# Kernel tuning notes

Hardware: AMD Instinct MI355X
Metric: run time of the kernel (lower is better)

## Reference

```python
import jax, jax.numpy as jnp
import numpy as np

HID = 128
SCALE = np.sqrt(HID)


def _ln(x, g, b, eps=1e-5):
    m = jnp.mean(x, axis=-1, keepdims=True)
    v = jnp.mean((x - m) ** 2, axis=-1, keepdims=True)
    return (x - m) * jax.lax.rsqrt(v + eps) * g + b


def _attention(img, txt, Wi, bi, Wt, bt, g1, b1, Wq, bq, Wk, bk, Wv, bv, g2, b2, Wo, bo):
    # img: [..., S, image_dim], txt: [..., S, text_dim] -> [..., S, HID]
    c = img @ Wi.T + bi + txt @ Wt.T + bt
    c = _ln(c, g1, b1)
    q = c @ Wq.T + bq
    k = c @ Wk.T + bk
    v = c @ Wv.T + bv
    s = jnp.einsum('...qd,...kd->...qk', q, k) / (SCALE + 1e-8)
    a = jax.nn.softmax(s, axis=-1)
    a = a + 1e-10
    a = a / jnp.sum(a, axis=-1, keepdims=True)
    a = jnp.clip(a, 1e-7, 1.0)
    ctx = jnp.einsum('...qk,...kd->...qd', a, v)
    ctx = _ln(ctx, g2, b2)
    return ctx @ Wo.T + bo


def setup_inputs() -> dict:
    key = jax.random.key(0)
    ks = jax.random.split(key, 24)
    T, Q, DI, DT = 256, 64, 2048, 768

    def xavier(k, shape):
        fan_in, fan_out = shape[1], shape[0]
        lim = np.sqrt(6.0 / (fan_in + fan_out))
        return jax.random.uniform(k, shape, jnp.float32, -lim, lim)

    return {
        'support_images': jax.random.normal(ks[0], (T, 4, DI), jnp.float32),
        'support_texts': jax.random.normal(ks[1], (T, 4, DT), jnp.float32),
        'support_labels': jax.random.randint(ks[2], (T, 4), 0, 4, jnp.int64),
        'query_images': jax.random.normal(ks[3], (T, Q, DI), jnp.float32),
        'query_texts': jax.random.normal(ks[4], (T, Q, DT), jnp.float32),
        'Wi': xavier(ks[5], (HID, DI)), 'bi': jnp.zeros((HID,)),
        'Wt': xavier(ks[6], (HID, DT)), 'bt': jnp.zeros((HID,)),
        'g1': jnp.ones((HID,)), 'b1': jnp.zeros((HID,)),
        'Wq': xavier(ks[7], (HID, HID)), 'bq': jnp.zeros((HID,)),
        'Wk': xavier(ks[8], (HID, HID)), 'bk': jnp.zeros((HID,)),
        'Wv': xavier(ks[9], (HID, HID)), 'bv': jnp.zeros((HID,)),
        'g2': jnp.ones((HID,)), 'b2': jnp.zeros((HID,)),
        'Wo': xavier(ks[10], (HID, HID)), 'bo': jnp.zeros((HID,)),
    }


def reference(support_images, support_texts, support_labels, query_images, query_texts,
              Wi, bi, Wt, bt, g1, b1, Wq, bq, Wk, bk, Wv, bv, g2, b2, Wo, bo):
    p = (Wi, bi, Wt, bt, g1, b1, Wq, bq, Wk, bk, Wv, bv, g2, b2, Wo, bo)
    # Support: attention across the 4 support items of each task -> [T, 4, HID]
    support_feats = _attention(support_images, support_texts, *p)
    # Queries: source processes each query alone (seq len 1) -> add singleton seq axis
    qf = _attention(query_images[:, :, None, :], query_texts[:, :, None, :], *p)
    qf = qf[:, :, 0, :]  # [T, Q, HID]
    # Cosine-similarity prototype scoring (eps=1e-8 as in F.cosine_similarity)
    qn = qf / jnp.clip(jnp.linalg.norm(qf, axis=-1, keepdims=True), 1e-8, None)
    pn = support_feats / jnp.clip(jnp.linalg.norm(support_feats, axis=-1, keepdims=True), 1e-8, None)
    logits = jnp.einsum('tqd,tcd->tqc', qn, pn) * 10.0  # [T, Q, 4]
    return logits
```

## Files before the change

### kernel.cpp

```cpp
#include <hip/hip_runtime.h>

typedef __bf16 bf16_t;
typedef __attribute__((ext_vector_type(4))) __bf16 bf16x4;
typedef __attribute__((ext_vector_type(8))) __bf16 bf16x8;
typedef __attribute__((ext_vector_type(4))) float floatx4;

#define LN_EPS 1e-5f

__global__ __launch_bounds__(256) void k0_init(
    const float* __restrict__ bi, const float* __restrict__ bt,
    float* __restrict__ c_all)
{
    int i = blockIdx.x * 256 + threadIdx.x;
    int c4 = i & 31;
    float4 a = ((const float4*)bi)[c4];
    float4 b = ((const float4*)bt)[c4];
    float4 v; v.x = a.x + b.x; v.y = a.y + b.y; v.z = a.z + b.z; v.w = a.w + b.w;
    ((float4*)c_all)[i] = v;
}

#define K1_SA 72
#define K1_SB 72

__global__ __launch_bounds__(256) void k1_gemm(
    const float* __restrict__ qimg, const float* __restrict__ qtxt,
    const float* __restrict__ simg, const float* __restrict__ stxt,
    const float* __restrict__ Wi,   const float* __restrict__ Wt,
    float* __restrict__ c_all)
{
    __shared__ bf16_t lA[64 * K1_SA];
    __shared__ bf16_t lB[128 * K1_SB];

    const int tid  = threadIdx.x;
    const int m0   = blockIdx.x * 64;
    const int chnk = blockIdx.y;
    const bool isq = (m0 < 16384);
    const int rb   = isq ? m0 : (m0 - 16384);
    const float* Aimg = isq ? qimg : simg;
    const float* Atxt = isq ? qtxt : stxt;

    const int wid  = tid >> 6;
    const int lane = tid & 63;
    const int quad = lane >> 4;
    const int l16  = lane & 15;
    const int wr   = wid >> 1;
    const int wc   = wid & 1;

    const int arow = tid >> 2, acol = (tid & 3) * 4;

    floatx4 acc[2][4];
#pragma unroll
    for (int i = 0; i < 2; ++i)
#pragma unroll
        for (int j = 0; j < 4; ++j) acc[i][j] = (floatx4)0.f;

    for (int s = 0; s < 11; ++s) {
        const int k0 = chnk * 704 + s * 64;
        const float* abase; const float* bbase; size_t lda, ldb;
        if (k0 < 2048) {
            abase = Aimg + (size_t)rb * 2048 + k0; lda = 2048;
            bbase = Wi + k0;                        ldb = 2048;
        } else {
            abase = Atxt + (size_t)rb * 768 + (k0 - 2048); lda = 768;
            bbase = Wt + (k0 - 2048);                       ldb = 768;
        }
        __syncthreads();
        {
            const float* p = abase + (size_t)arow * lda + acol;
#pragma unroll
            for (int j = 0; j < 4; ++j) {
                float4 v = *(const float4*)(p + 16 * j);
                bf16x4 pk; pk.x = (bf16_t)v.x; pk.y = (bf16_t)v.y;
                           pk.z = (bf16_t)v.z; pk.w = (bf16_t)v.w;
                *(bf16x4*)&lA[arow * K1_SA + acol + 16 * j] = pk;
            }
        }
#pragma unroll
        for (int pp = 0; pp < 2; ++pp) {
            int brow = pp * 64 + (tid >> 2);
            const float* p = bbase + (size_t)brow * ldb + acol;
#pragma unroll
            for (int j = 0; j < 4; ++j) {
                float4 v = *(const float4*)(p + 16 * j);
                bf16x4 pk; pk.x = (bf16_t)v.x; pk.y = (bf16_t)v.y;
                           pk.z = (bf16_t)v.z; pk.w = (bf16_t)v.w;
                *(bf16x4*)&lB[brow * K1_SB + acol + 16 * j] = pk;
            }
        }
        __syncthreads();
#pragma unroll
        for (int ks = 0; ks < 2; ++ks) {
            bf16x8 af[2], bfr[4];
#pragma unroll
            for (int mt = 0; mt < 2; ++mt)
                af[mt] = *(const bf16x8*)&lA[(wr * 32 + mt * 16 + l16) * K1_SA + ks * 32 + quad * 8];
#pragma unroll
            for (int nt = 0; nt < 4; ++nt)
                bfr[nt] = *(const bf16x8*)&lB[(wc * 64 + nt * 16 + l16) * K1_SB + ks * 32 + quad * 8];
#pragma unroll
            for (int mt = 0; mt < 2; ++mt)
#pragma unroll
                for (int nt = 0; nt < 4; ++nt)
                    acc[mt][nt] = __builtin_amdgcn_mfma_f32_16x16x32_bf16(
                        af[mt], bfr[nt], acc[mt][nt], 0, 0, 0);
        }
    }
#pragma unroll
    for (int nt = 0; nt < 4; ++nt) {
        int col = wc * 64 + nt * 16 + l16;
#pragma unroll
        for (int mt = 0; mt < 2; ++mt)
#pragma unroll
            for (int r = 0; r < 4; ++r) {
                int row = wr * 32 + mt * 16 + quad * 4 + r;
                unsafeAtomicAdd(&c_all[(size_t)(m0 + row) * 128 + col], acc[mt][nt][r]);
            }
    }
}

#define K2_ST 136

__global__ __launch_bounds__(256) void k2_query(
    const float* __restrict__ c_all,
    const float* __restrict__ Wv, const float* __restrict__ bv,
    const float* __restrict__ Wo, const float* __restrict__ bo,
    const float* __restrict__ g1, const float* __restrict__ b1,
    const float* __restrict__ g2, const float* __restrict__ b2,
    float* __restrict__ qn)
{
    __shared__ bf16_t tT[64 * K2_ST];
    __shared__ bf16_t tW[128 * K2_ST];

    const int tid  = threadIdx.x;
    const int wid  = tid >> 6;
    const int lane = tid & 63;
    const int quad = lane >> 4;
    const int l16  = lane & 15;
    const int t0   = blockIdx.x * 64;
    const int r0   = wid * 16;

    float bvr[8], g2r[8], b2r[8], bor[8];
#pragma unroll
    for (int nt = 0; nt < 8; ++nt) {
        int col = nt * 16 + l16;
        bvr[nt] = bv[col]; g2r[nt] = g2[col]; b2r[nt] = b2[col]; bor[nt] = bo[col];
    }
    const float g1l = g1[lane], g1h = g1[64 + lane];
    const float b1l = b1[lane], b1h = b1[64 + lane];

    for (int i = 0; i < 16; ++i) {
        int row = r0 + i;
        const float* src = c_all + (size_t)(t0 + row) * 128;
        float x0 = src[lane], x1 = src[64 + lane];
        float s = x0 + x1, q = x0 * x0 + x1 * x1;
#pragma unroll
        for (int m = 1; m < 64; m <<= 1) { s += __shfl_xor(s, m); q += __shfl_xor(q, m); }
        float mean = s * (1.f / 128.f);
        float var  = q * (1.f / 128.f) - mean * mean;
        float rs   = rsqrtf(var + LN_EPS);
        tT[row * K2_ST + lane]      = (bf16_t)((x0 - mean) * rs * g1l + b1l);
        tT[row * K2_ST + 64 + lane] = (bf16_t)((x1 - mean) * rs * g1h + b1h);
    }
#pragma unroll
    for (int i = 0; i < 16; ++i) {
        int idx = i * 1024 + tid * 4;
        int r = idx >> 7, cc = idx & 127;
        float4 v = *(const float4*)(Wv + idx);
        bf16x4 pk; pk.x = (bf16_t)v.x; pk.y = (bf16_t)v.y;
                   pk.z = (bf16_t)v.z; pk.w = (bf16_t)v.w;
        *(bf16x4*)&tW[r * K2_ST + cc] = pk;
    }
    __syncthreads();

    floatx4 acc[8];
#pragma unroll
    for (int nt = 0; nt < 8; ++nt) acc[nt] = (floatx4)0.f;
#pragma unroll
    for (int ks = 0; ks < 4; ++ks) {
        bf16x8 a = *(const bf16x8*)&tT[(r0 + l16) * K2_ST + ks * 32 + quad * 8];
#pragma unroll
        for (int nt = 0; nt < 8; ++nt) {
            bf16x8 b = *(const bf16x8*)&tW[(nt * 16 + l16) * K2_ST + ks * 32 + quad * 8];
            acc[nt] = __builtin_amdgcn_mfma_f32_16x16x32_bf16(a, b, acc[nt], 0, 0, 0);
        }
    }
#pragma unroll
    for (int nt = 0; nt < 8; ++nt)
#pragma unroll
        for (int r = 0; r < 4; ++r) acc[nt][r] += bvr[nt];

#pragma unroll
    for (int r = 0; r < 4; ++r) {
        float s = 0.f, q = 0.f;
#pragma unroll
        for (int nt = 0; nt < 8; ++nt) { float x = acc[nt][r]; s += x; q += x * x; }
#pragma unroll
        for (int m = 1; m < 16; m <<= 1) { s += __shfl_xor(s, m); q += __shfl_xor(q, m); }
        float mean = s * (1.f / 128.f);
        float var  = q * (1.f / 128.f) - mean * mean;
        float rs   = rsqrtf(var + LN_EPS);
        int row = r0 + quad * 4 + r;
#pragma unroll
        for (int nt = 0; nt < 8; ++nt) {
            float y = (acc[nt][r] - mean) * rs * g2r[nt] + b2r[nt];
            tT[row * K2_ST + nt * 16 + l16] = (bf16_t)y;
        }
    }
    __syncthreads();
#pragma unroll
    for (int i = 0; i < 16; ++i) {
        int idx = i * 1024 + tid * 4;
        int r = idx >> 7, cc = idx & 127;
        float4 v = *(const float4*)(Wo + idx);
        bf16x4 pk; pk.x = (bf16_t)v.x; pk.y = (bf16_t)v.y;
                   pk.z = (bf16_t)v.z; pk.w = (bf16_t)v.w;
        *(bf16x4*)&tW[r * K2_ST + cc] = pk;
    }
    __syncthreads();

#pragma unroll
    for (int nt = 0; nt < 8; ++nt) acc[nt] = (floatx4)0.f;
#pragma unroll
    for (int ks = 0; ks < 4; ++ks) {
        bf16x8 a = *(const bf16x8*)&tT[(r0 + l16) * K2_ST + ks * 32 + quad * 8];
#pragma unroll
        for (int nt = 0; nt < 8; ++nt) {
            bf16x8 b = *(const bf16x8*)&tW[(nt * 16 + l16) * K2_ST + ks * 32 + quad * 8];
            acc[nt] = __builtin_amdgcn_mfma_f32_16x16x32_bf16(a, b, acc[nt], 0, 0, 0);
        }
    }
#pragma unroll
    for (int r = 0; r < 4; ++r) {
        float q = 0.f;
#pragma unroll
        for (int nt = 0; nt < 8; ++nt) {
            float x = acc[nt][r] + bor[nt]; acc[nt][r] = x; q += x * x;
        }
#pragma unroll
        for (int m = 1; m < 16; m <<= 1) q += __shfl_xor(q, m);
        float inv = 1.f / fmaxf(sqrtf(q), 1e-8f);
        int row = t0 + r0 + quad * 4 + r;
#pragma unroll
        for (int nt = 0; nt < 8; ++nt)
            qn[(size_t)row * 128 + nt * 16 + l16] = acc[nt][r] * inv;
    }
}

__global__ __launch_bounds__(256) void k3_support(
    const float* __restrict__ c_all,
    const float* __restrict__ Wq, const float* __restrict__ bq,
    const float* __restrict__ Wk, const float* __restrict__ bk,
    const float* __restrict__ Wv, const float* __restrict__ bv,
    const float* __restrict__ Wo, const float* __restrict__ bo,
    const float* __restrict__ g1, const float* __restrict__ b1,
    const float* __restrict__ g2, const float* __restrict__ b2,
    float* __restrict__ pn)
{
    __shared__ float  cs[4][128];
    __shared__ bf16_t tW[128 * K2_ST];
    __shared__ float  qkv[3][4][128];
    __shared__ float  att[4][4];
    __shared__ float  ctx[4][128];

    const int tid  = threadIdx.x;
    const int wid  = tid >> 6;
    const int lane = tid & 63;
    const int task = blockIdx.x;

    {
        const float* src = c_all + (size_t)(16384 + task * 4 + wid) * 128;
        float x0 = src[lane], x1 = src[64 + lane];
        float s = x0 + x1, q = x0 * x0 + x1 * x1;
#pragma unroll
        for (int m = 1; m < 64; m <<= 1) { s += __shfl_xor(s, m); q += __shfl_xor(q, m); }
        float mean = s * (1.f / 128.f);
        float var  = q * (1.f / 128.f) - mean * mean;
        float rs   = rsqrtf(var + LN_EPS);
        cs[wid][lane]      = (x0 - mean) * rs * g1[lane] + b1[lane];
        cs[wid][64 + lane] = (x1 - mean) * rs * g1[64 + lane] + b1[64 + lane];
    }

    const float* Ws[3] = { Wq, Wk, Wv };
    const float* Bs[3] = { bq, bk, bv };
    for (int w = 0; w < 3; ++w) {
        __syncthreads();
#pragma unroll
        for (int i = 0; i < 16; ++i) {
            int idx = i * 1024 + tid * 4;
            int r = idx >> 7, cc = idx & 127;
            float4 v = *(const float4*)(Ws[w] + idx);
            bf16x4 pk; pk.x = (bf16_t)v.x; pk.y = (bf16_t)v.y;
                       pk.z = (bf16_t)v.z; pk.w = (bf16_t)v.w;
            *(bf16x4*)&tW[r * K2_ST + cc] = pk;
        }
        __syncthreads();
#pragma unroll
        for (int j = 0; j < 2; ++j) {
            int o = tid + j * 256;
            int s = o >> 7, n = o & 127;
            const float4* c4 = (const float4*)cs[s];
            float acc = 0.f;
#pragma unroll
            for (int k8 = 0; k8 < 16; ++k8) {
                bf16x8 wv = *(const bf16x8*)&tW[n * K2_ST + k8 * 8];
                float4 a0 = c4[k8 * 2], a1 = c4[k8 * 2 + 1];
                acc += a0.x * (float)wv[0] + a0.y * (float)wv[1]
                     + a0.z * (float)wv[2] + a0.w * (float)wv[3]
                     + a1.x * (float)wv[4] + a1.y * (float)wv[5]
                     + a1.z * (float)wv[6] + a1.w * (float)wv[7];
            }
            qkv[w][s][n] = acc + Bs[w][n];
        }
    }
    __syncthreads();
    if (tid < 16) {
        int i = tid >> 2, j = tid & 3;
        const float4* qv = (const float4*)qkv[0][i];
        const float4* kv = (const float4*)qkv[1][j];
        float acc = 0.f;
#pragma unroll
        for (int k = 0; k < 32; ++k) {
            float4 a = qv[k], b = kv[k];
            acc += a.x * b.x + a.y * b.y + a.z * b.z + a.w * b.w;
        }
        att[i][j] = acc * (float)(1.0 / (11.313708498984761 + 1e-8));
    }
    __syncthreads();
    if (tid < 4) {
        float s0 = att[tid][0], s1 = att[tid][1], s2 = att[tid][2], s3 = att[tid][3];
        float m = fmaxf(fmaxf(s0, s1), fmaxf(s2, s3));
        float e0 = expf(s0 - m), e1 = expf(s1 - m), e2 = expf(s2 - m), e3 = expf(s3 - m);
        float se = e0 + e1 + e2 + e3;
        float a0 = e0 / se + 1e-10f, a1 = e1 / se + 1e-10f;
        float a2 = e2 / se + 1e-10f, a3 = e3 / se + 1e-10f;
        float t = a0 + a1 + a2 + a3;
        att[tid][0] = fminf(fmaxf(a0 / t, 1e-7f), 1.f);
        att[tid][1] = fminf(fmaxf(a1 / t, 1e-7f), 1.f);
        att[tid][2] = fminf(fmaxf(a2 / t, 1e-7f), 1.f);
        att[tid][3] = fminf(fmaxf(a3 / t, 1e-7f), 1.f);
    }
    __syncthreads();
#pragma unroll
    for (int j = 0; j < 2; ++j) {
        int o = tid + j * 256;
        int s = o >> 7, n = o & 127;
        ctx[s][n] = att[s][0] * qkv[2][0][n] + att[s][1] * qkv[2][1][n]
                  + att[s][2] * qkv[2][2][n] + att[s][3] * qkv[2][3][n];
    }
    __syncthreads();
    {
        float x0 = ctx[wid][lane], x1 = ctx[wid][64 + lane];
        float s = x0 + x1, q = x0 * x0 + x1 * x1;
#pragma unroll
        for (int m = 1; m < 64; m <<= 1) { s += __shfl_xor(s, m); q += __shfl_xor(q, m); }
        float mean = s * (1.f / 128.f);
        float var  = q * (1.f / 128.f) - mean * mean;
        float rs   = rsqrtf(var + LN_EPS);
        cs[wid][lane]      = (x0 - mean) * rs * g2[lane] + b2[lane];
        cs[wid][64 + lane] = (x1 - mean) * rs * g2[64 + lane] + b2[64 + lane];
    }
    __syncthreads();
#pragma unroll
    for (int i = 0; i < 16; ++i) {
        int idx = i * 1024 + tid * 4;
        int r = idx >> 7, cc = idx & 127;
        float4 v = *(const float4*)(Wo + idx);
        bf16x4 pk; pk.x = (bf16_t)v.x; pk.y = (bf16_t)v.y;
                   pk.z = (bf16_t)v.z; pk.w = (bf16_t)v.w;
        *(bf16x4*)&tW[r * K2_ST + cc] = pk;
    }
    __syncthreads();
#pragma unroll
    for (int j = 0; j < 2; ++j) {
        int o = tid + j * 256;
        int s = o >> 7, n = o & 127;
        const float4* c4 = (const float4*)cs[s];
        float acc = 0.f;
#pragma unroll
        for (int k8 = 0; k8 < 16; ++k8) {
            bf16x8 wv = *(const bf16x8*)&tW[n * K2_ST + k8 * 8];
            float4 a0 = c4[k8 * 2], a1 = c4[k8 * 2 + 1];
            acc += a0.x * (float)wv[0] + a0.y * (float)wv[1]
                 + a0.z * (float)wv[2] + a0.w * (float)wv[3]
                 + a1.x * (float)wv[4] + a1.y * (float)wv[5]
                 + a1.z * (float)wv[6] + a1.w * (float)wv[7];
        }
        ctx[s][n] = acc + bo[n];
    }
    __syncthreads();
    {
        float x0 = ctx[wid][lane], x1 = ctx[wid][64 + lane];
        float q = x0 * x0 + x1 * x1;
#pragma unroll
        for (int m = 1; m < 64; m <<= 1) q += __shfl_xor(q, m);
        float inv = 1.f / fmaxf(sqrtf(q), 1e-8f);
        float* dst = pn + (size_t)(task * 4 + wid) * 128;
        dst[lane]      = x0 * inv;
        dst[64 + lane] = x1 * inv;
    }
}

__global__ __launch_bounds__(256) void k4_logits(
    const float* __restrict__ qn, const float* __restrict__ pn,
    float* __restrict__ out)
{
    __shared__ float qs[64][132];
    __shared__ float ps[4][132];
    const int tid  = threadIdx.x;
    const int task = blockIdx.x;
#pragma unroll
    for (int j = 0; j < 8; ++j) {
        int i = tid + 256 * j;
        int r = i >> 5, c = (i & 31) * 4;
        *(float4*)&qs[r][c] = *(const float4*)(qn + ((size_t)task * 64 + r) * 128 + c);
    }
    if (tid < 128) {
        int r = tid >> 5, c = (tid & 31) * 4;
        *(float4*)&ps[r][c] = *(const float4*)(pn + ((size_t)task * 4 + r) * 128 + c);
    }
    __syncthreads();
    const int qi = tid >> 2, cc = tid & 3;
    const float4* q4 = (const float4*)qs[qi];
    const float4* p4 = (const float4*)ps[cc];
    float acc = 0.f;
#pragma unroll
    for (int k = 0; k < 32; ++k) {
        float4 a = q4[k], b = p4[k];
        acc += a.x * b.x + a.y * b.y + a.z * b.z + a.w * b.w;
    }
    out[(size_t)task * 256 + qi * 4 + cc] = acc * 10.f;
}

extern "C" void kernel_launch(void* const* d_in, const int* in_sizes, int n_in,
                              void* d_out, int out_size, void* d_ws, size_t ws_size,
                              hipStream_t stream)
{
    const float* simg = (const float*)d_in[0];
    const float* stxt = (const float*)d_in[1];
    const float* qimg = (const float*)d_in[3];
    const float* qtxt = (const float*)d_in[4];
    const float* Wi = (const float*)d_in[5];
    const float* bi = (const float*)d_in[6];
    const float* Wt = (const float*)d_in[7];
    const float* bt = (const float*)d_in[8];
    const float* g1 = (const float*)d_in[9];
    const float* b1 = (const float*)d_in[10];
    const float* Wq = (const float*)d_in[11];
    const float* bq = (const float*)d_in[12];
    const float* Wk = (const float*)d_in[13];
    const float* bk = (const float*)d_in[14];
    const float* Wv = (const float*)d_in[15];
    const float* bv = (const float*)d_in[16];
    const float* g2 = (const float*)d_in[17];
    const float* b2 = (const float*)d_in[18];
    const float* Wo = (const float*)d_in[19];
    const float* bo = (const float*)d_in[20];
    float* out = (float*)d_out;

    float* c_all = (float*)d_ws;
    float* qn    = c_all + (size_t)17408 * 128;
    float* pn    = qn    + (size_t)16384 * 128;

    k0_init<<<2176, 256, 0, stream>>>(bi, bt, c_all);
    k1_gemm<<<dim3(272, 4), 256, 0, stream>>>(qimg, qtxt, simg, stxt, Wi, Wt, c_all);
    k2_query<<<256, 256, 0, stream>>>(c_all, Wv, bv, Wo, bo, g1, b1, g2, b2, qn);
    k3_support<<<256, 256, 0, stream>>>(c_all, Wq, bq, Wk, bk, Wv, bv, Wo, bo,
                                        g1, b1, g2, b2, pn);
    k4_logits<<<256, 256, 0, stream>>>(qn, pn, out);
}
```

Baseline: 384.8 us.

## Use direct global-to-LDS loads, pre-convert weights, fuse logits into query kernel

The main GEMM now loads fp32 tiles straight into LDS through global_load_lds with an XOR swizzle and converts them to bf16 at fragment-read time. It uses a 32-wide K step and sets an occupancy hint. The small 128x128 weights are converted to bf16 once in the prep kernel, then streamed into swizzled LDS by the support and query kernels. The logits kernel is folded into the query kernel, which now runs after the support kernel and dots against the normalized prototypes directly. This drops one launch and the qn round trip. The cost is fp32 LDS tiles, twice as many K-loop iterations with barriers, and conversion work repeated inside the inner loop.

```diff
diff --git a/kernel.cpp b/kernel.cpp
--- a/kernel.cpp
+++ b/kernel.cpp
@@ -7,29 +7,46 @@
 
 #define LN_EPS 1e-5f
 
-__global__ __launch_bounds__(256) void k0_init(
+__device__ __forceinline__ void dma16(const void* g, void* l) {
+    __builtin_amdgcn_global_load_lds(
+        (const __attribute__((address_space(1))) void*)g,
+        (__attribute__((address_space(3))) void*)l, 16, 0, 0);
+}
+
+__global__ __launch_bounds__(256) void k0_prep(
     const float* __restrict__ bi, const float* __restrict__ bt,
-    float* __restrict__ c_all)
+    const float* __restrict__ Wq, const float* __restrict__ Wk,
+    const float* __restrict__ Wv, const float* __restrict__ Wo,
+    float* __restrict__ c_all, bf16_t* __restrict__ wbf)
 {
-    int i = blockIdx.x * 256 + threadIdx.x;
-    int c4 = i & 31;
-    float4 a = ((const float4*)bi)[c4];
-    float4 b = ((const float4*)bt)[c4];
-    float4 v; v.x = a.x + b.x; v.y = a.y + b.y; v.z = a.z + b.z; v.w = a.w + b.w;
-    ((float4*)c_all)[i] = v;
-}
-
-#define K1_SA 72
-#define K1_SB 72
-
-__global__ __launch_bounds__(256) void k1_gemm(
+    const int b = blockIdx.x;
+    if (b < 2176) {
+        int i = b * 256 + threadIdx.x;
+        int c4 = i & 31;
+        float4 a = ((const float4*)bi)[c4];
+        float4 bb = ((const float4*)bt)[c4];
+        float4 v; v.x = a.x + bb.x; v.y = a.y + bb.y; v.z = a.z + bb.z; v.w = a.w + bb.w;
+        ((float4*)c_all)[i] = v;
+    } else {
+        int i4 = (b - 2176) * 256 + threadIdx.x;
+        int which = i4 >> 12;
+        int off4  = i4 & 4095;
+        const float* W = (which == 0) ? Wq : (which == 1) ? Wk : (which == 2) ? Wv : Wo;
+        float4 v = ((const float4*)W)[off4];
+        bf16x4 pk; pk.x = (bf16_t)v.x; pk.y = (bf16_t)v.y;
+                   pk.z = (bf16_t)v.z; pk.w = (bf16_t)v.w;
+        *(bf16x4*)&wbf[which * 16384 + off4 * 4] = pk;
+    }
+}
+
+__global__ __launch_bounds__(256, 4) void k1_gemm(
     const float* __restrict__ qimg, const float* __restrict__ qtxt,
     const float* __restrict__ simg, const float* __restrict__ stxt,
     const float* __restrict__ Wi,   const float* __restrict__ Wt,
     float* __restrict__ c_all)
 {
-    __shared__ bf16_t lA[64 * K1_SA];
-    __shared__ bf16_t lB[128 * K1_SB];
+    __shared__ float lA[64 * 32];
+    __shared__ float lB[128 * 32];
 
     const int tid  = threadIdx.x;
     const int m0   = blockIdx.x * 64;
@@ -46,7 +63,8 @@
     const int wr   = wid >> 1;
     const int wc   = wid & 1;
 
-    const int arow = tid >> 2, acol = (tid & 3) * 4;
+    const int jr = lane >> 3;
+    const int cA = (lane & 7) ^ jr;
 
     floatx4 acc[2][4];
 #pragma unroll
@@ -54,8 +72,8 @@
 #pragma unroll
         for (int j = 0; j < 4; ++j) acc[i][j] = (floatx4)0.f;
 
-    for (int s = 0; s < 11; ++s) {
-        const int k0 = chnk * 704 + s * 64;
+    for (int s = 0; s < 22; ++s) {
+        const int k0 = chnk * 704 + s * 32;
         const float* abase; const float* bbase; size_t lda, ldb;
         if (k0 < 2048) {
             abase = Aimg + (size_t)rb * 2048 + k0; lda = 2048;
@@ -65,45 +83,48 @@
             bbase = Wt + (k0 - 2048);                       ldb = 768;
         }
         __syncthreads();
-        {
-            const float* p = abase + (size_t)arow * lda + acol;
-#pragma unroll
-            for (int j = 0; j < 4; ++j) {
-                float4 v = *(const float4*)(p + 16 * j);
-                bf16x4 pk; pk.x = (bf16_t)v.x; pk.y = (bf16_t)v.y;
-                           pk.z = (bf16_t)v.z; pk.w = (bf16_t)v.w;
-                *(bf16x4*)&lA[arow * K1_SA + acol + 16 * j] = pk;
-            }
-        }
-#pragma unroll
-        for (int pp = 0; pp < 2; ++pp) {
-            int brow = pp * 64 + (tid >> 2);
-            const float* p = bbase + (size_t)brow * ldb + acol;
-#pragma unroll
-            for (int j = 0; j < 4; ++j) {
-                float4 v = *(const float4*)(p + 16 * j);
-                bf16x4 pk; pk.x = (bf16_t)v.x; pk.y = (bf16_t)v.y;
-                           pk.z = (bf16_t)v.z; pk.w = (bf16_t)v.w;
-                *(bf16x4*)&lB[brow * K1_SB + acol + 16 * j] = pk;
-            }
+#pragma unroll
+        for (int ii = 0; ii < 2; ++ii) {
+            int i = 2 * wid + ii;
+            dma16(abase + (size_t)(8 * i + jr) * lda + (cA << 2),
+                  (char*)lA + i * 1024);
+        }
+#pragma unroll
+        for (int ii = 0; ii < 4; ++ii) {
+            int i = 4 * wid + ii;
+            dma16(bbase + (size_t)(8 * i + jr) * ldb + (cA << 2),
+                  (char*)lB + i * 1024);
         }
         __syncthreads();
-#pragma unroll
-        for (int ks = 0; ks < 2; ++ks) {
-            bf16x8 af[2], bfr[4];
-#pragma unroll
-            for (int mt = 0; mt < 2; ++mt)
-                af[mt] = *(const bf16x8*)&lA[(wr * 32 + mt * 16 + l16) * K1_SA + ks * 32 + quad * 8];
+
+        const int x7 = l16 & 7;
+        bf16x8 af[2], bfr[4];
+#pragma unroll
+        for (int mt = 0; mt < 2; ++mt) {
+            int R = wr * 32 + mt * 16 + l16;
+            float4 f0 = *(const float4*)&lA[R * 32 + (((2 * quad)     ^ x7) << 2)];
+            float4 f1 = *(const float4*)&lA[R * 32 + (((2 * quad + 1) ^ x7) << 2)];
+            bf16x8 a;
+            a[0] = (bf16_t)f0.x; a[1] = (bf16_t)f0.y; a[2] = (bf16_t)f0.z; a[3] = (bf16_t)f0.w;
+            a[4] = (bf16_t)f1.x; a[5] = (bf16_t)f1.y; a[6] = (bf16_t)f1.z; a[7] = (bf16_t)f1.w;
+            af[mt] = a;
+        }
+#pragma unroll
+        for (int nt = 0; nt < 4; ++nt) {
+            int R = wc * 64 + nt * 16 + l16;
+            float4 f0 = *(const float4*)&lB[R * 32 + (((2 * quad)     ^ x7) << 2)];
+            float4 f1 = *(const float4*)&lB[R * 32 + (((2 * quad + 1) ^ x7) << 2)];
+            bf16x8 b;
+            b[0] = (bf16_t)f0.x; b[1] = (bf16_t)f0.y; b[2] = (bf16_t)f0.z; b[3] = (bf16_t)f0.w;
+            b[4] = (bf16_t)f1.x; b[5] = (bf16_t)f1.y; b[6] = (bf16_t)f1.z; b[7] = (bf16_t)f1.w;
+            bfr[nt] = b;
+        }
+#pragma unroll
+        for (int mt = 0; mt < 2; ++mt)
 #pragma unroll
             for (int nt = 0; nt < 4; ++nt)
-                bfr[nt] = *(const bf16x8*)&lB[(wc * 64 + nt * 16 + l16) * K1_SB + ks * 32 + quad * 8];
-#pragma unroll
-            for (int mt = 0; mt < 2; ++mt)
-#pragma unroll
-                for (int nt = 0; nt < 4; ++nt)
-                    acc[mt][nt] = __builtin_amdgcn_mfma_f32_16x16x32_bf16(
-                        af[mt], bfr[nt], acc[mt][nt], 0, 0, 0);
-        }
+                acc[mt][nt] = __builtin_amdgcn_mfma_f32_16x16x32_bf16(
+                    af[mt], bfr[nt], acc[mt][nt], 0, 0, 0);
     }
 #pragma unroll
     for (int nt = 0; nt < 4; ++nt) {
@@ -121,23 +142,41 @@
 #define K2_ST 136
 
 __global__ __launch_bounds__(256) void k2_query(
-    const float* __restrict__ c_all,
-    const float* __restrict__ Wv, const float* __restrict__ bv,
-    const float* __restrict__ Wo, const float* __restrict__ bo,
+    const float* __restrict__ c_all, const bf16_t* __restrict__ wbf,
+    const float* __restrict__ bv, const float* __restrict__ bo,
     const float* __restrict__ g1, const float* __restrict__ b1,
     const float* __restrict__ g2, const float* __restrict__ b2,
-    float* __restrict__ qn)
+    const float* __restrict__ pn, float* __restrict__ out)
 {
     __shared__ bf16_t tT[64 * K2_ST];
-    __shared__ bf16_t tW[128 * K2_ST];
+    __shared__ bf16_t tW[128 * 128];
+    __shared__ float  pl[4][132];
 
     const int tid  = threadIdx.x;
     const int wid  = tid >> 6;
     const int lane = tid & 63;
     const int quad = lane >> 4;
     const int l16  = lane & 15;
-    const int t0   = blockIdx.x * 64;
+    const int task = blockIdx.x;
+    const int t0   = task * 64;
     const int r0   = wid * 16;
+
+    const bf16_t* Wvb = wbf + 2 * 16384;
+    const bf16_t* Wob = wbf + 3 * 16384;
+
+    const int jr4 = lane >> 4;
+    const int jp  = lane & 15;
+#pragma unroll
+    for (int ii = 0; ii < 8; ++ii) {
+        int i = 8 * wid + ii;
+        int row = 4 * i + jr4;
+        int c = jp ^ (row & 15);
+        dma16(Wvb + row * 128 + c * 8, (char*)tW + i * 1024);
+    }
+    if (tid < 128) {
+        int r = tid >> 5, c4 = tid & 31;
+        *(float4*)&pl[r][c4 * 4] = *(const float4*)(pn + ((size_t)task * 4 + r) * 128 + c4 * 4);
+    }
 
     float bvr[8], g2r[8], b2r[8], bor[8];
 #pragma unroll
@@ -145,30 +184,37 @@
         int col = nt * 16 + l16;
         bvr[nt] = bv[col]; g2r[nt] = g2[col]; b2r[nt] = b2[col]; bor[nt] = bo[col];
     }
-    const float g1l = g1[lane], g1h = g1[64 + lane];
-    const float b1l = b1[lane], b1h = b1[64 + lane];
-
-    for (int i = 0; i < 16; ++i) {
-        int row = r0 + i;
-        const float* src = c_all + (size_t)(t0 + row) * 128;
-        float x0 = src[lane], x1 = src[64 + lane];
-        float s = x0 + x1, q = x0 * x0 + x1 * x1;
-#pragma unroll
-        for (int m = 1; m < 64; m <<= 1) { s += __shfl_xor(s, m); q += __shfl_xor(q, m); }
+
+    const int g8 = lane >> 3;
+    const int s8 = lane & 7;
+    float g1a[16], b1a[16];
+#pragma unroll
+    for (int mm = 0; mm < 4; ++mm) {
+        *(float4*)&g1a[mm * 4] = ((const float4*)(g1 + s8 * 16))[mm];
+        *(float4*)&b1a[mm * 4] = ((const float4*)(b1 + s8 * 16))[mm];
+    }
+#pragma unroll
+    for (int p = 0; p < 2; ++p) {
+        int rloc = r0 + p * 8 + g8;
+        const float* src = c_all + (size_t)(t0 + rloc) * 128 + s8 * 16;
+        float v[16];
+#pragma unroll
+        for (int mm = 0; mm < 4; ++mm) *(float4*)&v[mm * 4] = ((const float4*)src)[mm];
+        float s = 0.f, q = 0.f;
+#pragma unroll
+        for (int m = 0; m < 16; ++m) { s += v[m]; q += v[m] * v[m]; }
+#pragma unroll
+        for (int m = 1; m < 8; m <<= 1) { s += __shfl_xor(s, m); q += __shfl_xor(q, m); }
         float mean = s * (1.f / 128.f);
         float var  = q * (1.f / 128.f) - mean * mean;
         float rs   = rsqrtf(var + LN_EPS);
-        tT[row * K2_ST + lane]      = (bf16_t)((x0 - mean) * rs * g1l + b1l);
-        tT[row * K2_ST + 64 + lane] = (bf16_t)((x1 - mean) * rs * g1h + b1h);
-    }
-#pragma unroll
-    for (int i = 0; i < 16; ++i) {
-        int idx = i * 1024 + tid * 4;
-        int r = idx >> 7, cc = idx & 127;
-        float4 v = *(const float4*)(Wv + idx);
-        bf16x4 pk; pk.x = (bf16_t)v.x; pk.y = (bf16_t)v.y;
-                   pk.z = (bf16_t)v.z; pk.w = (bf16_t)v.w;
-        *(bf16x4*)&tW[r * K2_ST + cc] = pk;
+        bf16x8 o0, o1;
+#pragma unroll
+        for (int m = 0; m < 8; ++m)  o0[m] = (bf16_t)((v[m] - mean) * rs * g1a[m] + b1a[m]);
+#pragma unroll
+        for (int m = 0; m < 8; ++m)  o1[m] = (bf16_t)((v[8 + m] - mean) * rs * g1a[8 + m] + b1a[8 + m]);
+        *(bf16x8*)&tT[rloc * K2_ST + s8 * 16]     = o0;
+        *(bf16x8*)&tT[rloc * K2_ST + s8 * 16 + 8] = o1;
     }
     __syncthreads();
 
@@ -180,7 +226,7 @@
         bf16x8 a = *(const bf16x8*)&tT[(r0 + l16) * K2_ST + ks * 32 + quad * 8];
 #pragma unroll
         for (int nt = 0; nt < 8; ++nt) {
-            bf16x8 b = *(const bf16x8*)&tW[(nt * 16 + l16) * K2_ST + ks * 32 + quad * 8];
+            bf16x8 b = *(const bf16x8*)&tW[(nt * 16 + l16) * 128 + (((ks * 4 + quad) ^ l16) << 3)];
             acc[nt] = __builtin_amdgcn_mfma_f32_16x16x32_bf16(a, b, acc[nt], 0, 0, 0);
         }
     }
@@ -201,20 +247,16 @@
         float rs   = rsqrtf(var + LN_EPS);
         int row = r0 + quad * 4 + r;
 #pragma unroll
-        for (int nt = 0; nt < 8; ++nt) {
-            float y = (acc[nt][r] - mean) * rs * g2r[nt] + b2r[nt];
-            tT[row * K2_ST + nt * 16 + l16] = (bf16_t)y;
-        }
-    }
-    __syncthreads();
-#pragma unroll
-    for (int i = 0; i < 16; ++i) {
-        int idx = i * 1024 + tid * 4;
-        int r = idx >> 7, cc = idx & 127;
-        float4 v = *(const float4*)(Wo + idx);
-        bf16x4 pk; pk.x = (bf16_t)v.x; pk.y = (bf16_t)v.y;
-                   pk.z = (bf16_t)v.z; pk.w = (bf16_t)v.w;
-        *(bf16x4*)&tW[r * K2_ST + cc] = pk;
+        for (int nt = 0; nt < 8; ++nt)
+            tT[row * K2_ST + nt * 16 + l16] = (bf16_t)((acc[nt][r] - mean) * rs * g2r[nt] + b2r[nt]);
+    }
+    __syncthreads();
+#pragma unroll
+    for (int ii = 0; ii < 8; ++ii) {
+        int i = 8 * wid + ii;
+        int row = 4 * i + jr4;
+        int c = jp ^ (row & 15);
+        dma16(Wob + row * 128 + c * 8, (char*)tW + i * 1024);
     }
     __syncthreads();
 
@@ -225,39 +267,52 @@
         bf16x8 a = *(const bf16x8*)&tT[(r0 + l16) * K2_ST + ks * 32 + quad * 8];
 #pragma unroll
         for (int nt = 0; nt < 8; ++nt) {
-            bf16x8 b = *(const bf16x8*)&tW[(nt * 16 + l16) * K2_ST + ks * 32 + quad * 8];
+            bf16x8 b = *(const bf16x8*)&tW[(nt * 16 + l16) * 128 + (((ks * 4 + quad) ^ l16) << 3)];
             acc[nt] = __builtin_amdgcn_mfma_f32_16x16x32_bf16(a, b, acc[nt], 0, 0, 0);
         }
     }
+
 #pragma unroll
     for (int r = 0; r < 4; ++r) {
-        float q = 0.f;
+        float st[8]; float q = 0.f;
 #pragma unroll
         for (int nt = 0; nt < 8; ++nt) {
-            float x = acc[nt][r] + bor[nt]; acc[nt][r] = x; q += x * x;
+            float x = acc[nt][r] + bor[nt]; st[nt] = x; q += x * x;
         }
 #pragma unroll
         for (int m = 1; m < 16; m <<= 1) q += __shfl_xor(q, m);
         float inv = 1.f / fmaxf(sqrtf(q), 1e-8f);
-        int row = t0 + r0 + quad * 4 + r;
-#pragma unroll
-        for (int nt = 0; nt < 8; ++nt)
-            qn[(size_t)row * 128 + nt * 16 + l16] = acc[nt][r] * inv;
+        float d0 = 0.f, d1 = 0.f, d2 = 0.f, d3 = 0.f;
+#pragma unroll
+        for (int nt = 0; nt < 8; ++nt) {
+            float xn = st[nt] * inv;
+            int col = nt * 16 + l16;
+            d0 += xn * pl[0][col]; d1 += xn * pl[1][col];
+            d2 += xn * pl[2][col]; d3 += xn * pl[3][col];
+        }
+#pragma unroll
+        for (int m = 1; m < 16; m <<= 1) {
+            d0 += __shfl_xor(d0, m); d1 += __shfl_xor(d1, m);
+            d2 += __shfl_xor(d2, m); d3 += __shfl_xor(d3, m);
+        }
+        if (l16 == 0) {
+            int qi = r0 + quad * 4 + r;
+            float* o = out + (size_t)task * 256 + qi * 4;
+            o[0] = d0 * 10.f; o[1] = d1 * 10.f; o[2] = d2 * 10.f; o[3] = d3 * 10.f;
+        }
     }
 }
 
 __global__ __launch_bounds__(256) void k3_support(
-    const float* __restrict__ c_all,
-    const float* __restrict__ Wq, const float* __restrict__ bq,
-    const float* __restrict__ Wk, const float* __restrict__ bk,
-    const float* __restrict__ Wv, const float* __restrict__ bv,
-    const float* __restrict__ Wo, const float* __restrict__ bo,
+    const float* __restrict__ c_all, const bf16_t* __restrict__ wbf,
+    const float* __restrict__ bq, const float* __restrict__ bk,
+    const float* __restrict__ bv, const float* __restrict__ bo,
     const float* __restrict__ g1, const float* __restrict__ b1,
     const float* __restrict__ g2, const float* __restrict__ b2,
     float* __restrict__ pn)
 {
     __shared__ float  cs[4][128];
-    __shared__ bf16_t tW[128 * K2_ST];
+    __shared__ bf16_t tW[128 * 128];
     __shared__ float  qkv[3][4][128];
     __shared__ float  att[4][4];
     __shared__ float  ctx[4][128];
@@ -266,6 +321,8 @@
     const int wid  = tid >> 6;
     const int lane = tid & 63;
     const int task = blockIdx.x;
+    const int jr4  = lane >> 4;
+    const int jp   = lane & 15;
 
     {
         const float* src = c_all + (size_t)(16384 + task * 4 + wid) * 128;
@@ -280,18 +337,15 @@
         cs[wid][64 + lane] = (x1 - mean) * rs * g1[64 + lane] + b1[64 + lane];
     }
 
-    const float* Ws[3] = { Wq, Wk, Wv };
     const float* Bs[3] = { bq, bk, bv };
     for (int w = 0; w < 3; ++w) {
         __syncthreads();
 #pragma unroll
-        for (int i = 0; i < 16; ++i) {
-            int idx = i * 1024 + tid * 4;
-            int r = idx >> 7, cc = idx & 127;
-            float4 v = *(const float4*)(Ws[w] + idx);
-            bf16x4 pk; pk.x = (bf16_t)v.x; pk.y = (bf16_t)v.y;
-                       pk.z = (bf16_t)v.z; pk.w = (bf16_t)v.w;
-            *(bf16x4*)&tW[r * K2_ST + cc] = pk;
+        for (int ii = 0; ii < 8; ++ii) {
+            int i = 8 * wid + ii;
+            int row = 4 * i + jr4;
+            int c = jp ^ (row & 15);
+            dma16(wbf + w * 16384 + row * 128 + c * 8, (char*)tW + i * 1024);
         }
         __syncthreads();
 #pragma unroll
@@ -301,9 +355,9 @@
             const float4* c4 = (const float4*)cs[s];
             float acc = 0.f;
 #pragma unroll
-            for (int k8 = 0; k8 < 16; ++k8) {
-                bf16x8 wv = *(const bf16x8*)&tW[n * K2_ST + k8 * 8];
-                float4 a0 = c4[k8 * 2], a1 = c4[k8 * 2 + 1];
+            for (int c = 0; c < 16; ++c) {
+                bf16x8 wv = *(const bf16x8*)&tW[n * 128 + ((c ^ (n & 15)) << 3)];
+                float4 a0 = c4[c * 2], a1 = c4[c * 2 + 1];
                 acc += a0.x * (float)wv[0] + a0.y * (float)wv[1]
                      + a0.z * (float)wv[2] + a0.w * (float)wv[3]
                      + a1.x * (float)wv[4] + a1.y * (float)wv[5]
@@ -361,13 +415,11 @@
     }
     __syncthreads();
 #pragma unroll
-    for (int i = 0; i < 16; ++i) {
-        int idx = i * 1024 + tid * 4;
-        int r = idx >> 7, cc = idx & 127;
-        float4 v = *(const float4*)(Wo + idx);
-        bf16x4 pk; pk.x = (bf16_t)v.x; pk.y = (bf16_t)v.y;
-                   pk.z = (bf16_t)v.z; pk.w = (bf16_t)v.w;
-        *(bf16x4*)&tW[r * K2_ST + cc] = pk;
+    for (int ii = 0; ii < 8; ++ii) {
+        int i = 8 * wid + ii;
+        int row = 4 * i + jr4;
+        int c = jp ^ (row & 15);
+        dma16(wbf + 3 * 16384 + row * 128 + c * 8, (char*)tW + i * 1024);
     }
     __syncthreads();
 #pragma unroll
@@ -377,9 +429,9 @@
         const float4* c4 = (const float4*)cs[s];
         float acc = 0.f;
 #pragma unroll
-        for (int k8 = 0; k8 < 16; ++k8) {
-            bf16x8 wv = *(const bf16x8*)&tW[n * K2_ST + k8 * 8];
-            float4 a0 = c4[k8 * 2], a1 = c4[k8 * 2 + 1];
+        for (int c = 0; c < 16; ++c) {
+            bf16x8 wv = *(const bf16x8*)&tW[n * 128 + ((c ^ (n & 15)) << 3)];
+            float4 a0 = c4[c * 2], a1 = c4[c * 2 + 1];
             acc += a0.x * (float)wv[0] + a0.y * (float)wv[1]
                  + a0.z * (float)wv[2] + a0.w * (float)wv[3]
                  + a1.x * (float)wv[4] + a1.y * (float)wv[5]
@@ -398,37 +450,6 @@
         dst[lane]      = x0 * inv;
         dst[64 + lane] = x1 * inv;
     }
-}
-
-__global__ __launch_bounds__(256) void k4_logits(
-    const float* __restrict__ qn, const float* __restrict__ pn,
-    float* __restrict__ out)
-{
-    __shared__ float qs[64][132];
-    __shared__ float ps[4][132];
-    const int tid  = threadIdx.x;
-    const int task = blockIdx.x;
-#pragma unroll
-    for (int j = 0; j < 8; ++j) {
-        int i = tid + 256 * j;
-        int r = i >> 5, c = (i & 31) * 4;
-        *(float4*)&qs[r][c] = *(const float4*)(qn + ((size_t)task * 64 + r) * 128 + c);
-    }
-    if (tid < 128) {
-        int r = tid >> 5, c = (tid & 31) * 4;
-        *(float4*)&ps[r][c] = *(const float4*)(pn + ((size_t)task * 4 + r) * 128 + c);
-    }
-    __syncthreads();
-    const int qi = tid >> 2, cc = tid & 3;
-    const float4* q4 = (const float4*)qs[qi];
-    const float4* p4 = (const float4*)ps[cc];
-    float acc = 0.f;
-#pragma unroll
-    for (int k = 0; k < 32; ++k) {
-        float4 a = q4[k], b = p4[k];
-        acc += a.x * b.x + a.y * b.y + a.z * b.z + a.w * b.w;
-    }
-    out[(size_t)task * 256 + qi * 4 + cc] = acc * 10.f;
 }
 
 extern "C" void kernel_launch(void* const* d_in, const int* in_sizes, int n_in,
@@ -457,14 +478,12 @@
     const float* bo = (const float*)d_in[20];
     float* out = (float*)d_out;
 
-    float* c_all = (float*)d_ws;
-    float* qn    = c_all + (size_t)17408 * 128;
-    float* pn    = qn    + (size_t)16384 * 128;
-
-    k0_init<<<2176, 256, 0, stream>>>(bi, bt, c_all);
+    float*  c_all = (float*)d_ws;
+    float*  pn    = c_all + (size_t)17408 * 128;
+    bf16_t* wbf   = (bf16_t*)(pn + (size_t)1024 * 128);
+
+    k0_prep<<<2240, 256, 0, stream>>>(bi, bt, Wq, Wk, Wv, Wo, c_all, wbf);
     k1_gemm<<<dim3(272, 4), 256, 0, stream>>>(qimg, qtxt, simg, stxt, Wi, Wt, c_all);
-    k2_query<<<256, 256, 0, stream>>>(c_all, Wv, bv, Wo, bo, g1, b1, g2, b2, qn);
-    k3_support<<<256, 256, 0, stream>>>(c_all, Wq, bq, Wk, bk, Wv, bv, Wo, bo,
-                                        g1, b1, g2, b2, pn);
-    k4_logits<<<256, 256, 0, stream>>>(qn, pn, out);
-}
+    k3_support<<<256, 256, 0, stream>>>(c_all, wbf, bq, bk, bv, bo, g1, b1, g2, b2, pn);
+    k2_query<<<256, 256, 0, stream>>>(c_all, wbf, bv, bo, g1, b1, g2, b2, pn, out);
+}
```

Result: faster. 325.6 us (-15.4%).
